# Performance work log

Measured on AMD Instinct MI355X. Metric: run time of the kernel, lower is better.

Reference implementation:

```python
import jax, jax.numpy as jnp
import numpy as np

TAU = 0.5

def setup_inputs() -> dict:
    key = jax.random.key(0)
    ks = jax.random.split(key, 8)
    B_Nq, B_Ns, C, H, W = 16, 16, 512, 32, 32
    f_q = jax.random.normal(ks[0], (B_Nq, C, H, W), dtype=jnp.float32)
    f_s = jax.random.normal(ks[1], (B_Ns, C, H, W), dtype=jnp.float32)
    # depthwise 1x1 convs with groups=dim, bias=False -> per-channel scalar weights [C]
    w_cca_q = jax.random.normal(ks[2], (C,), dtype=jnp.float32)
    w_cca_k = jax.random.normal(ks[3], (C,), dtype=jnp.float32)
    w_cca_v = jax.random.normal(ks[4], (C,), dtype=jnp.float32)
    w_sca_q = jax.random.normal(ks[5], (C,), dtype=jnp.float32)
    w_sca_k = jax.random.normal(ks[6], (C,), dtype=jnp.float32)
    lam = jnp.float32(0.1)
    return {"f_q": f_q, "f_s": f_s, "w_cca_q": w_cca_q, "w_cca_k": w_cca_k,
            "w_cca_v": w_cca_v, "w_sca_q": w_sca_q, "w_sca_k": w_sca_k, "lam": lam}

def _dw(x, w):
    # depthwise 1x1 conv, no bias == per-channel scale; x: [B,C,H,W], w: [C]
    return x * w[None, :, None, None]

def reference(f_q, f_s, w_cca_q, w_cca_k, w_cca_v, w_sca_q, w_sca_k, lam):
    B_Nq, C, H, W = f_q.shape
    B_Ns = f_s.shape[0]
    P = H * W
    qc = _dw(f_q, w_cca_q).reshape(B_Nq, C, P)          # [B,C,P]
    kc_mean = _dw(f_s, w_cca_k).reshape(B_Ns, C, P).mean(axis=0)  # [C,P]
    vc_mean = _dw(f_s, w_cca_v).reshape(B_Ns, C, P).mean(axis=0)  # [C,P]
    # channel attention: [B,C,C]
    Ac = jax.nn.softmax(jnp.einsum('bcp,dp->bcd', qc, kc_mean) / P, axis=-1)
    f_cca_q = jnp.einsum('bcd,dp->bcp', Ac, vc_mean).reshape(B_Nq, C, H, W)
    qs = _dw(f_cca_q, w_sca_q).reshape(B_Nq, C, P)      # [B,C,P]
    ks_mean = _dw(f_s, w_sca_k).reshape(B_Ns, C, P).mean(axis=0)  # [C,P]
    # spatial affinity: [B,P,P]
    M = jnp.einsum('bcp,cq->bpq', qs, ks_mean) / (TAU * C)
    alpha = jax.nn.softmax(M.mean(axis=-1), axis=-1)    # [B_Nq,P]
    beta = jax.nn.softmax(M.mean(axis=-2), axis=-1)     # [B_Nq,P]
    beta_mean = jnp.broadcast_to(beta.mean(axis=0, keepdims=True), (B_Ns, P))
    Fq_out = f_q + lam * f_cca_q
    return (Fq_out, alpha, beta_mean)
```

## Files before the change

### kernel.cpp

```cpp
#include <hip/hip_runtime.h>

typedef __bf16 bf16;
typedef __bf16 bf16x4 __attribute__((ext_vector_type(4)));
typedef __bf16 bf16x8 __attribute__((ext_vector_type(8)));
typedef float f32x4 __attribute__((ext_vector_type(4)));


#define GLL16(g, l)                                                             \
    __builtin_amdgcn_global_load_lds((const __attribute__((address_space(1))) void*)(g), \
                                     (__attribute__((address_space(3))) void*)(l), 16, 0, 0)

__device__ inline float wave_reduce_sum(float v) {
#pragma unroll
    for (int m = 32; m >= 1; m >>= 1) v += __shfl_xor(v, m, 64);
    return v;
}
__device__ inline float wave_reduce_max(float v) {
#pragma unroll
    for (int m = 32; m >= 1; m >>= 1) v = fmaxf(v, __shfl_xor(v, m, 64));
    return v;
}

__global__ void k_prep(const float* __restrict__ fs, const float* __restrict__ fq,
                       float* __restrict__ fsm32, bf16* __restrict__ fsm16,
                       bf16* __restrict__ fsmT, bf16* __restrict__ fq16) {
    __shared__ bf16 tile[32][33];
    int bx = blockIdx.x, by = blockIdx.y;
    int p0 = bx * 32, c0 = by * 32;
    int t = threadIdx.x, tx = t & 31, ty = t >> 5;
#pragma unroll
    for (int i = 0; i < 4; ++i) {
        size_t off = (size_t)(c0 + ty + 8 * i) * 1024 + p0 + tx;
        float s = 0.f;
#pragma unroll
        for (int b = 0; b < 16; ++b) s += fs[(size_t)b * 524288 + off];
        s *= (1.f / 16.f);
        fsm32[off] = s;
        bf16 h = (bf16)s;
        fsm16[off] = h;
        tile[ty + 8 * i][tx] = h;
    }
    __syncthreads();
#pragma unroll
    for (int i = 0; i < 4; ++i)
        fsmT[(size_t)(p0 + ty + 8 * i) * 512 + c0 + tx] = tile[tx][ty + 8 * i];
    int blk = by * 32 + bx;
    const float4* f4 = (const float4*)fq;
#pragma unroll
    for (int i = 0; i < 16; ++i) {
        int idx = blk * 4096 + i * 256 + t;
        float4 v = f4[idx];
        bf16x4 h4 = {(bf16)v.x, (bf16)v.y, (bf16)v.z, (bf16)v.w};
        *(bf16x4*)(fq16 + (size_t)idx * 4) = h4;
    }
}

__global__ void k_u(const float* __restrict__ fsm32, const float* __restrict__ wsq,
                    const float* __restrict__ wsk, float* __restrict__ u,
                    float* __restrict__ rm) {
    int c = blockIdx.x;
    int t = threadIdx.x;
    float s = 0.f;
#pragma unroll
    for (int j = 0; j < 4; ++j) s += fsm32[(size_t)c * 1024 + t + 256 * j];
    s = wave_reduce_sum(s);
    __shared__ float red[4];
    int w = t >> 6, lane = t & 63;
    if (lane == 0) red[w] = s;
    __syncthreads();
    if (t == 0) {
        float rmv = (red[0] + red[1] + red[2] + red[3]) * (1.f / 1024.f);
        rm[c] = rmv;
        u[c] = wsq[c] * wsk[c] * rmv * (1.f / 256.f);
    }
}

__global__ void k_gemm1(const bf16* __restrict__ A, const bf16* __restrict__ B,
                        float* __restrict__ G) {
    __shared__ alignas(16) bf16 As[64 * 32];
    __shared__ alignas(16) bf16 Bs[128 * 32];
    const int dt = blockIdx.x, ct = blockIdx.y, b = blockIdx.z;
    const int t = threadIdx.x, w = t >> 6, lane = t & 63;
    const int quad = lane >> 4, r15 = lane & 15;
    const bf16* Abase = A + ((size_t)(b * 512 + ct * 64)) * 1024;
    const bf16* Bbase = B + ((size_t)(dt * 128)) * 1024;
    const int sr = t >> 2, sc = (t & 3) * 8;
    f32x4 acc[8] = {};
    for (int k0 = 0; k0 < 1024; k0 += 32) {
        GLL16(Abase + (size_t)sr * 1024 + k0 + sc, As + t * 8);
        GLL16(Bbase + (size_t)sr * 1024 + k0 + sc, Bs + t * 8);
        GLL16(Bbase + (size_t)(sr + 64) * 1024 + k0 + sc, Bs + (t + 256) * 8);
        __syncthreads();
        bf16x8 af = *(const bf16x8*)(As + (w * 16 + r15) * 32 + quad * 8);
#pragma unroll
        for (int j = 0; j < 8; ++j) {
            bf16x8 bfr = *(const bf16x8*)(Bs + (j * 16 + r15) * 32 + quad * 8);
            acc[j] = __builtin_amdgcn_mfma_f32_16x16x32_bf16(af, bfr, acc[j], 0, 0, 0);
        }
        __syncthreads();
    }
    float* g = G + ((size_t)(b * 512 + ct * 64 + w * 16 + quad * 4)) * 512 + dt * 128 + r15;
#pragma unroll
    for (int j = 0; j < 8; ++j)
#pragma unroll
        for (int ii = 0; ii < 4; ++ii)
            g[(size_t)ii * 512 + j * 16] = acc[j][ii];
}

__global__ void k_softmax_ac(const float* __restrict__ G, const float* __restrict__ wq,
                             const float* __restrict__ wk, const float* __restrict__ wv,
                             const float* __restrict__ rm, bf16* __restrict__ Acw,
                             float* __restrict__ r) {
    int row = blockIdx.x * 4 + (threadIdx.x >> 6);
    int lane = threadIdx.x & 63;
    int c = row & 511;
    const float* g = G + (size_t)row * 512;
    float sc = wq[c] * (1.f / 1024.f);
    float v[8];
    float mx = -3.4e38f;
#pragma unroll
    for (int j = 0; j < 8; ++j) {
        int d = lane + 64 * j;
        v[j] = g[d] * sc * wk[d];
        mx = fmaxf(mx, v[j]);
    }
    mx = wave_reduce_max(mx);
    float sum = 0.f;
#pragma unroll
    for (int j = 0; j < 8; ++j) {
        v[j] = __expf(v[j] - mx);
        sum += v[j];
    }
    sum = wave_reduce_sum(sum);
    float inv = 1.f / sum;
    bf16* o = Acw + (size_t)row * 512;
    float rsum = 0.f;
#pragma unroll
    for (int j = 0; j < 8; ++j) {
        int d = lane + 64 * j;
        float aw = v[j] * inv * wv[d];
        o[d] = (bf16)aw;
        rsum += aw * rm[d];
    }
    rsum = wave_reduce_sum(rsum);
    if (lane == 0) r[row] = rsum;
}

__global__ void k_t(const bf16* __restrict__ Acw, const float* __restrict__ u,
                    float* __restrict__ tbp) {
    int half = blockIdx.z, b = blockIdx.y;
    int d = blockIdx.x * 256 + threadIdx.x;
    const bf16* base = Acw + (size_t)b * 262144 + (size_t)half * 256 * 512 + d;
    const float* uu = u + half * 256;
    float s = 0.f;
#pragma unroll 16
    for (int c = 0; c < 256; ++c) s += uu[c] * (float)base[(size_t)c * 512];
    tbp[(half * 16 + b) * 512 + d] = s;
}

__global__ void k_gemm2(const bf16* __restrict__ A, const bf16* __restrict__ B,
                        const float* __restrict__ fq, const float* __restrict__ lamp,
                        float* __restrict__ out) {
    __shared__ alignas(16) bf16 As[64 * 32];
    __shared__ alignas(16) bf16 Bs[128 * 32];
    const int pt = blockIdx.x, ct = blockIdx.y, b = blockIdx.z;
    const int t = threadIdx.x, w = t >> 6, lane = t & 63;
    const int quad = lane >> 4, r15 = lane & 15;
    const bf16* Abase = A + ((size_t)(b * 512 + ct * 64)) * 512;
    const bf16* Bbase = B + ((size_t)(pt * 128)) * 512;
    const int sr = t >> 2, sc = (t & 3) * 8;
    f32x4 acc[8] = {};
    for (int k0 = 0; k0 < 512; k0 += 32) {
        GLL16(Abase + (size_t)sr * 512 + k0 + sc, As + t * 8);
        GLL16(Bbase + (size_t)sr * 512 + k0 + sc, Bs + t * 8);
        GLL16(Bbase + (size_t)(sr + 64) * 512 + k0 + sc, Bs + (t + 256) * 8);
        __syncthreads();
        bf16x8 af = *(const bf16x8*)(As + (w * 16 + r15) * 32 + quad * 8);
#pragma unroll
        for (int j = 0; j < 8; ++j) {
            bf16x8 bfr = *(const bf16x8*)(Bs + (j * 16 + r15) * 32 + quad * 8);
            acc[j] = __builtin_amdgcn_mfma_f32_16x16x32_bf16(af, bfr, acc[j], 0, 0, 0);
        }
        __syncthreads();
    }
    float lam = lamp[0];
    size_t rowbase = (size_t)(b * 512 + ct * 64 + w * 16 + quad * 4);
#pragma unroll
    for (int j = 0; j < 8; ++j)
#pragma unroll
        for (int ii = 0; ii < 4; ++ii) {
            size_t idx = (rowbase + ii) * 1024 + pt * 128 + j * 16 + r15;
            out[idx] = fq[idx] + lam * acc[j][ii];
        }
}

__global__ void k_logits(const float* __restrict__ tbp, const float* __restrict__ r,
                         const float* __restrict__ wsq, const float* __restrict__ wsk,
                         const float* __restrict__ fsm32, float* __restrict__ alog,
                         float* __restrict__ blog) {
    int z = blockIdx.y, pq = blockIdx.x * 256 + threadIdx.x;
    if (z < 16) {
        const float* t0 = tbp + z * 512;
        const float* t1 = tbp + (16 + z) * 512;
        float s = 0.f;
#pragma unroll 8
        for (int d = 0; d < 512; ++d) s += (t0[d] + t1[d]) * fsm32[(size_t)d * 1024 + pq];
        alog[z * 1024 + pq] = s;
    } else {
        int b = z - 16;
        float s = 0.f;
#pragma unroll 8
        for (int c = 0; c < 512; ++c) {
            float coef = r[b * 512 + c] * wsq[c] * wsk[c] * (1.f / 256.f);
            s += coef * fsm32[(size_t)c * 1024 + pq];
        }
        blog[b * 1024 + pq] = s;
    }
}

__global__ void k_softmax_rows(const float* __restrict__ alog, const float* __restrict__ blog,
                               float* __restrict__ alpha_out, float* __restrict__ beta) {
    int z = blockIdx.x;
    int t = threadIdx.x;
    int w = t >> 6, lane = t & 63;
    const float* src = (z < 16) ? (alog + (size_t)z * 1024) : (blog + (size_t)(z - 16) * 1024);
    float v[4];
    float mx = -3.4e38f;
#pragma unroll
    for (int j = 0; j < 4; ++j) {
        v[j] = src[t + 256 * j];
        mx = fmaxf(mx, v[j]);
    }
    __shared__ float red[4];
    float wm = wave_reduce_max(mx);
    if (lane == 0) red[w] = wm;
    __syncthreads();
    mx = fmaxf(fmaxf(red[0], red[1]), fmaxf(red[2], red[3]));
    float s = 0.f;
#pragma unroll
    for (int j = 0; j < 4; ++j) {
        v[j] = __expf(v[j] - mx);
        s += v[j];
    }
    __syncthreads();
    float ws_ = wave_reduce_sum(s);
    if (lane == 0) red[w] = ws_;
    __syncthreads();
    s = red[0] + red[1] + red[2] + red[3];
    float inv = 1.f / s;
    if (z < 16) {
#pragma unroll
        for (int j = 0; j < 4; ++j) alpha_out[(size_t)z * 1024 + t + 256 * j] = v[j] * inv;
    } else {
#pragma unroll
        for (int j = 0; j < 4; ++j) beta[(size_t)(z - 16) * 1024 + t + 256 * j] = v[j] * inv;
    }
}

__global__ void k_betamean(const float* __restrict__ beta, float* __restrict__ out) {
    int q = blockIdx.x * 256 + threadIdx.x;
    float s = 0.f;
#pragma unroll
    for (int b = 0; b < 16; ++b) s += beta[b * 1024 + q];
    float val = s * (1.f / 16.f);
#pragma unroll
    for (int si = 0; si < 16; ++si) out[(size_t)si * 1024 + q] = val;
}

extern "C" void kernel_launch(void* const* d_in, const int* in_sizes, int n_in,
                              void* d_out, int out_size, void* d_ws, size_t ws_size,
                              hipStream_t stream) {
    const float* f_q = (const float*)d_in[0];
    const float* f_s = (const float*)d_in[1];
    const float* w_cca_q = (const float*)d_in[2];
    const float* w_cca_k = (const float*)d_in[3];
    const float* w_cca_v = (const float*)d_in[4];
    const float* w_sca_q = (const float*)d_in[5];
    const float* w_sca_k = (const float*)d_in[6];
    const float* lamp = (const float*)d_in[7];

    char* ws = (char*)d_ws;
    float* fsm32 = (float*)(ws + 0);
    bf16* fsm16 = (bf16*)(ws + 2097152);
    bf16* fsmT = (bf16*)(ws + 3145728);
    float* G = (float*)(ws + 4194304);
    bf16* Acw = (bf16*)(ws + 20971520);
    bf16* fq16 = (bf16*)(ws + 29360128);
    float* rm = (float*)(ws + 46137344);
    float* u = (float*)(ws + 46139392);
    float* r = (float*)(ws + 46141440);
    float* tbp = (float*)(ws + 46174208);
    float* alog = (float*)(ws + 46239744);
    float* blog = (float*)(ws + 46305280);
    float* beta = (float*)(ws + 46370816);

    float* out_fq = (float*)d_out;
    float* out_alpha = out_fq + 8388608;
    float* out_bmean = out_fq + 8404992;

    k_prep<<<dim3(32, 16), 256, 0, stream>>>(f_s, f_q, fsm32, fsm16, fsmT, fq16);
    k_u<<<512, 256, 0, stream>>>(fsm32, w_sca_q, w_sca_k, u, rm);
    k_gemm1<<<dim3(4, 8, 16), 256, 0, stream>>>(fq16, fsm16, G);
    k_softmax_ac<<<2048, 256, 0, stream>>>(G, w_cca_q, w_cca_k, w_cca_v, rm, Acw, r);
    k_t<<<dim3(2, 16, 2), 256, 0, stream>>>(Acw, u, tbp);
    k_gemm2<<<dim3(8, 8, 16), 256, 0, stream>>>(Acw, fsmT, f_q, lamp, out_fq);
    k_logits<<<dim3(4, 32), 256, 0, stream>>>(tbp, r, w_sca_q, w_sca_k, fsm32, alog, blog);
    k_softmax_rows<<<32, 256, 0, stream>>>(alog, blog, out_alpha, beta);
    k_betamean<<<4, 256, 0, stream>>>(beta, out_bmean);
}
```

Baseline: 204.1 us.

## Use 2x4 wave MFMA tiling with XOR-swizzled LDS and split reduction accumulators

Both bf16 GEMM kernels change their wave layout from 1x8 to a 2x2 wave grid, each wave computing a 2x4 block of 16x16 MFMA tiles. This raises fragment reuse and cuts LDS reads per MFMA. The LDS staging layout is XOR-swizzled on both the global_load_lds write side and the fragment read side, to avoid bank conflicts. The reduction loops in k_t and k_logits now use four independent accumulators to break the serial FMA dependency chain, which slightly changes floating-point summation order.

```diff
diff --git a/kernel.cpp b/kernel.cpp
--- a/kernel.cpp
+++ b/kernel.cpp
@@ -82,29 +82,47 @@
     const int dt = blockIdx.x, ct = blockIdx.y, b = blockIdx.z;
     const int t = threadIdx.x, w = t >> 6, lane = t & 63;
     const int quad = lane >> 4, r15 = lane & 15;
+    const int wr = w & 1, wc = w >> 1;
     const bf16* Abase = A + ((size_t)(b * 512 + ct * 64)) * 1024;
     const bf16* Bbase = B + ((size_t)(dt * 128)) * 1024;
-    const int sr = t >> 2, sc = (t & 3) * 8;
-    f32x4 acc[8] = {};
+    const int pr = t >> 2;
+    const int gc = (t & 3) ^ ((pr >> 1) & 3);
+    f32x4 acc[2][4] = {};
     for (int k0 = 0; k0 < 1024; k0 += 32) {
-        GLL16(Abase + (size_t)sr * 1024 + k0 + sc, As + t * 8);
-        GLL16(Bbase + (size_t)sr * 1024 + k0 + sc, Bs + t * 8);
-        GLL16(Bbase + (size_t)(sr + 64) * 1024 + k0 + sc, Bs + (t + 256) * 8);
+        GLL16(Abase + (size_t)pr * 1024 + k0 + gc * 8, As + t * 8);
+        GLL16(Bbase + (size_t)pr * 1024 + k0 + gc * 8, Bs + t * 8);
+        GLL16(Bbase + (size_t)(pr + 64) * 1024 + k0 + gc * 8, Bs + (t + 256) * 8);
         __syncthreads();
-        bf16x8 af = *(const bf16x8*)(As + (w * 16 + r15) * 32 + quad * 8);
-#pragma unroll
-        for (int j = 0; j < 8; ++j) {
-            bf16x8 bfr = *(const bf16x8*)(Bs + (j * 16 + r15) * 32 + quad * 8);
-            acc[j] = __builtin_amdgcn_mfma_f32_16x16x32_bf16(af, bfr, acc[j], 0, 0, 0);
-        }
+        bf16x8 af[2], bfr[4];
+#pragma unroll
+        for (int mi = 0; mi < 2; ++mi) {
+            int R = wr * 32 + mi * 16 + r15;
+            int sc = quad ^ ((R >> 1) & 3);
+            af[mi] = *(const bf16x8*)(As + R * 32 + sc * 8);
+        }
+#pragma unroll
+        for (int j = 0; j < 4; ++j) {
+            int R = wc * 64 + j * 16 + r15;
+            int sc = quad ^ ((R >> 1) & 3);
+            bfr[j] = *(const bf16x8*)(Bs + R * 32 + sc * 8);
+        }
+#pragma unroll
+        for (int mi = 0; mi < 2; ++mi)
+#pragma unroll
+            for (int j = 0; j < 4; ++j)
+                acc[mi][j] = __builtin_amdgcn_mfma_f32_16x16x32_bf16(af[mi], bfr[j], acc[mi][j], 0, 0, 0);
         __syncthreads();
     }
-    float* g = G + ((size_t)(b * 512 + ct * 64 + w * 16 + quad * 4)) * 512 + dt * 128 + r15;
-#pragma unroll
-    for (int j = 0; j < 8; ++j)
-#pragma unroll
-        for (int ii = 0; ii < 4; ++ii)
-            g[(size_t)ii * 512 + j * 16] = acc[j][ii];
+#pragma unroll
+    for (int mi = 0; mi < 2; ++mi) {
+        float* g = G + ((size_t)(b * 512 + ct * 64 + wr * 32 + mi * 16 + quad * 4)) * 512 +
+                   dt * 128 + wc * 64 + r15;
+#pragma unroll
+        for (int j = 0; j < 4; ++j)
+#pragma unroll
+            for (int ii = 0; ii < 4; ++ii)
+                g[(size_t)ii * 512 + j * 16] = acc[mi][j][ii];
+    }
 }
 
 __global__ void k_softmax_ac(const float* __restrict__ G, const float* __restrict__ wq,
@@ -152,10 +170,15 @@
     int d = blockIdx.x * 256 + threadIdx.x;
     const bf16* base = Acw + (size_t)b * 262144 + (size_t)half * 256 * 512 + d;
     const float* uu = u + half * 256;
-    float s = 0.f;
-#pragma unroll 16
-    for (int c = 0; c < 256; ++c) s += uu[c] * (float)base[(size_t)c * 512];
-    tbp[(half * 16 + b) * 512 + d] = s;
+    float s0 = 0.f, s1 = 0.f, s2 = 0.f, s3 = 0.f;
+#pragma unroll 4
+    for (int c = 0; c < 256; c += 4) {
+        s0 += uu[c] * (float)base[(size_t)c * 512];
+        s1 += uu[c + 1] * (float)base[(size_t)(c + 1) * 512];
+        s2 += uu[c + 2] * (float)base[(size_t)(c + 2) * 512];
+        s3 += uu[c + 3] * (float)base[(size_t)(c + 3) * 512];
+    }
+    tbp[(half * 16 + b) * 512 + d] = (s0 + s1) + (s2 + s3);
 }
 
 __global__ void k_gemm2(const bf16* __restrict__ A, const bf16* __restrict__ B,
@@ -166,32 +189,49 @@
     const int pt = blockIdx.x, ct = blockIdx.y, b = blockIdx.z;
     const int t = threadIdx.x, w = t >> 6, lane = t & 63;
     const int quad = lane >> 4, r15 = lane & 15;
+    const int wr = w & 1, wc = w >> 1;
     const bf16* Abase = A + ((size_t)(b * 512 + ct * 64)) * 512;
     const bf16* Bbase = B + ((size_t)(pt * 128)) * 512;
-    const int sr = t >> 2, sc = (t & 3) * 8;
-    f32x4 acc[8] = {};
+    const int pr = t >> 2;
+    const int gc = (t & 3) ^ ((pr >> 1) & 3);
+    f32x4 acc[2][4] = {};
     for (int k0 = 0; k0 < 512; k0 += 32) {
-        GLL16(Abase + (size_t)sr * 512 + k0 + sc, As + t * 8);
-        GLL16(Bbase + (size_t)sr * 512 + k0 + sc, Bs + t * 8);
-        GLL16(Bbase + (size_t)(sr + 64) * 512 + k0 + sc, Bs + (t + 256) * 8);
+        GLL16(Abase + (size_t)pr * 512 + k0 + gc * 8, As + t * 8);
+        GLL16(Bbase + (size_t)pr * 512 + k0 + gc * 8, Bs + t * 8);
+        GLL16(Bbase + (size_t)(pr + 64) * 512 + k0 + gc * 8, Bs + (t + 256) * 8);
         __syncthreads();
-        bf16x8 af = *(const bf16x8*)(As + (w * 16 + r15) * 32 + quad * 8);
-#pragma unroll
-        for (int j = 0; j < 8; ++j) {
-            bf16x8 bfr = *(const bf16x8*)(Bs + (j * 16 + r15) * 32 + quad * 8);
-            acc[j] = __builtin_amdgcn_mfma_f32_16x16x32_bf16(af, bfr, acc[j], 0, 0, 0);
-        }
+        bf16x8 af[2], bfr[4];
+#pragma unroll
+        for (int mi = 0; mi < 2; ++mi) {
+            int R = wr * 32 + mi * 16 + r15;
+            int sc = quad ^ ((R >> 1) & 3);
+            af[mi] = *(const bf16x8*)(As + R * 32 + sc * 8);
+        }
+#pragma unroll
+        for (int j = 0; j < 4; ++j) {
+            int R = wc * 64 + j * 16 + r15;
+            int sc = quad ^ ((R >> 1) & 3);
+            bfr[j] = *(const bf16x8*)(Bs + R * 32 + sc * 8);
+        }
+#pragma unroll
+        for (int mi = 0; mi < 2; ++mi)
+#pragma unroll
+            for (int j = 0; j < 4; ++j)
+                acc[mi][j] = __builtin_amdgcn_mfma_f32_16x16x32_bf16(af[mi], bfr[j], acc[mi][j], 0, 0, 0);
         __syncthreads();
     }
     float lam = lamp[0];
-    size_t rowbase = (size_t)(b * 512 + ct * 64 + w * 16 + quad * 4);
-#pragma unroll
-    for (int j = 0; j < 8; ++j)
-#pragma unroll
-        for (int ii = 0; ii < 4; ++ii) {
-            size_t idx = (rowbase + ii) * 1024 + pt * 128 + j * 16 + r15;
-            out[idx] = fq[idx] + lam * acc[j][ii];
-        }
+#pragma unroll
+    for (int mi = 0; mi < 2; ++mi) {
+        size_t rowbase = (size_t)(b * 512 + ct * 64 + wr * 32 + mi * 16 + quad * 4);
+#pragma unroll
+        for (int j = 0; j < 4; ++j)
+#pragma unroll
+            for (int ii = 0; ii < 4; ++ii) {
+                size_t idx = (rowbase + ii) * 1024 + pt * 128 + wc * 64 + j * 16 + r15;
+                out[idx] = fq[idx] + lam * acc[mi][j][ii];
+            }
+    }
 }
 
 __global__ void k_logits(const float* __restrict__ tbp, const float* __restrict__ r,
@@ -202,19 +242,27 @@
     if (z < 16) {
         const float* t0 = tbp + z * 512;
         const float* t1 = tbp + (16 + z) * 512;
-        float s = 0.f;
-#pragma unroll 8
-        for (int d = 0; d < 512; ++d) s += (t0[d] + t1[d]) * fsm32[(size_t)d * 1024 + pq];
-        alog[z * 1024 + pq] = s;
+        float s0 = 0.f, s1 = 0.f, s2 = 0.f, s3 = 0.f;
+#pragma unroll 2
+        for (int d = 0; d < 512; d += 4) {
+            s0 += (t0[d] + t1[d]) * fsm32[(size_t)d * 1024 + pq];
+            s1 += (t0[d + 1] + t1[d + 1]) * fsm32[(size_t)(d + 1) * 1024 + pq];
+            s2 += (t0[d + 2] + t1[d + 2]) * fsm32[(size_t)(d + 2) * 1024 + pq];
+            s3 += (t0[d + 3] + t1[d + 3]) * fsm32[(size_t)(d + 3) * 1024 + pq];
+        }
+        alog[z * 1024 + pq] = (s0 + s1) + (s2 + s3);
     } else {
         int b = z - 16;
-        float s = 0.f;
-#pragma unroll 8
-        for (int c = 0; c < 512; ++c) {
-            float coef = r[b * 512 + c] * wsq[c] * wsk[c] * (1.f / 256.f);
-            s += coef * fsm32[(size_t)c * 1024 + pq];
-        }
-        blog[b * 1024 + pq] = s;
+        const float* rb = r + b * 512;
+        float s0 = 0.f, s1 = 0.f, s2 = 0.f, s3 = 0.f;
+#pragma unroll 2
+        for (int c = 0; c < 512; c += 4) {
+            s0 += rb[c] * wsq[c] * wsk[c] * (1.f / 256.f) * fsm32[(size_t)c * 1024 + pq];
+            s1 += rb[c + 1] * wsq[c + 1] * wsk[c + 1] * (1.f / 256.f) * fsm32[(size_t)(c + 1) * 1024 + pq];
+            s2 += rb[c + 2] * wsq[c + 2] * wsk[c + 2] * (1.f / 256.f) * fsm32[(size_t)(c + 2) * 1024 + pq];
+            s3 += rb[c + 3] * wsq[c + 3] * wsk[c + 3] * (1.f / 256.f) * fsm32[(size_t)(c + 3) * 1024 + pq];
+        }
+        blog[b * 1024 + pq] = (s0 + s1) + (s2 + s3);
     }
 }
 
```

Result: no change. 202.6 us (-0.8%).
